# Kernel tuning notes

Measured on AMD Instinct MI355X. Metric: run time of the kernel, lower is better.

The kernel has to match this reference:

```python
import jax, jax.numpy as jnp
import numpy as np

IN_CAPS, IN_SIZE = 2401, 8
OUT_CAPS, OUT_SIZE = 8, 16
ROUTING_ITERS = 3


def squash(s, axis):
    mag_sq = jnp.sum(s * s, axis=axis, keepdims=True)
    mag = jnp.sqrt(mag_sq)
    return mag_sq / (1.0 + mag_sq) * (s / mag)


def setup_inputs() -> dict:
    key = jax.random.key(0)
    kx, kw = jax.random.split(key)
    B = 256
    x = jax.random.normal(kx, (B, IN_CAPS, IN_SIZE), dtype=jnp.float32)
    stdv = 1.0 / np.sqrt(IN_CAPS)
    W = jax.random.uniform(kw, (IN_CAPS, OUT_CAPS, OUT_SIZE, IN_SIZE),
                           dtype=jnp.float32, minval=-stdv, maxval=stdv)
    return {"x": x, "W": W}


def reference(x, W):
    # u_hat[b,i,o,c] = W[i,o,c,d] @ x[b,i,d]   -> [B, 2401, 8, 16]
    u_hat = jnp.einsum('iocd,bid->bioc', W, x)
    u_hat_det = jax.lax.stop_gradient(u_hat)

    b_ij = jnp.zeros((IN_CAPS, OUT_CAPS), dtype=x.dtype)
    v_j = None
    for it in range(ROUTING_ITERS):
        c_ij = jax.nn.softmax(b_ij, axis=1)  # softmax over out_capsules
        last = (it == ROUTING_ITERS - 1)
        u = u_hat if last else u_hat_det
        s_j = jnp.einsum('io,bioc->boc', c_ij, u)  # [B, 8, 16]
        v_j = squash(s_j, axis=-1)
        if not last:
            # agreement: mean over batch of <u_hat_i, v_j>
            a = jnp.einsum('bioc,boc->io', u_hat_det, v_j) / x.shape[0]
            b_ij = b_ij + a
    return v_j  # [B, 8, 16]
```

## Files before the change

kernel.cpp:

```cpp
#include <hip/hip_runtime.h>
#include <math.h>

#define IC     2401
#define BSZ    256
#define OC     8
#define CS     16
#define OCC    128
#define XROW   19208
#define KP     19264
#define KTILES 301
#define SNI    32

typedef __attribute__((ext_vector_type(8))) short short8;
typedef __attribute__((ext_vector_type(4))) float f32x4;

__device__ __forceinline__ unsigned short f2bf(float f) {
    union { float f; unsigned u; } v; v.f = f;
    const unsigned r = v.u + 0x7FFF + ((v.u >> 16) & 1);
    return (unsigned short)(r >> 16);
}
__device__ __forceinline__ float bf2f(unsigned short h) {
    union { unsigned u; float f; } v; v.u = ((unsigned)h) << 16;
    return v.f;
}
__device__ __forceinline__ void atomAddF32(float* p, float v) {
    (void)__hip_atomic_fetch_add(p, v, __ATOMIC_RELAXED, __HIP_MEMORY_SCOPE_AGENT);
}

__global__ __launch_bounds__(256)
void prep_kernel(const float* __restrict__ x, const float* __restrict__ W,
                 unsigned short* __restrict__ xT, unsigned short* __restrict__ xB,
                 unsigned short* __restrict__ Wbf, unsigned short* __restrict__ cwt,
                 float* __restrict__ s_acc_all)
{
    const int tid = threadIdx.x;
    if (blockIdx.x < 3) {
        float4* z = (float4*)(s_acc_all + (size_t)blockIdx.x * BSZ * OCC);
#pragma unroll
        for (int r = 0; r < 32; ++r)
            z[r * 256 + tid] = make_float4(0.f, 0.f, 0.f, 0.f);
    }
    if (blockIdx.x < 1204) {
        __shared__ float Ts[64 * 65];
        const int bg = blockIdx.x & 3;
        const int kt = blockIdx.x >> 2;
#pragma unroll
        for (int r = 0; r < 4; ++r) {
            const int flat = r * 256 + tid;
            const int b = flat >> 4, cq = flat & 15;
            const int col = kt * 64 + cq * 4;
            float4 v = make_float4(0.f, 0.f, 0.f, 0.f);
            if (col < XROW) v = *(const float4*)(x + (size_t)(bg * 64 + b) * XROW + col);
            *(float4*)&Ts[b * 65 + cq * 4] = v;
        }
        __syncthreads();
#pragma unroll
        for (int r = 0; r < 2; ++r) {
            const int flat = r * 256 + tid;
            const int rl = flat >> 3, bq = flat & 7;
            union { short8 v; unsigned short h[8]; } o;
#pragma unroll
            for (int j = 0; j < 8; ++j) o.h[j] = f2bf(Ts[(bq * 8 + j) * 65 + rl]);
            *(short8*)(xT + (size_t)(kt * 64 + rl) * 256 + bg * 64 + bq * 8) = o.v;
        }
#pragma unroll
        for (int r = 0; r < 2; ++r) {
            const int flat = r * 256 + tid;
            const int b = flat >> 3, g = flat & 7;
            union { short8 v; unsigned short h[8]; } o;
#pragma unroll
            for (int j = 0; j < 8; ++j) o.h[j] = f2bf(Ts[b * 65 + g * 8 + j]);
            *(short8*)(xB + (size_t)(bg * 64 + b) * KP + (size_t)kt * 64 + g * 8) = o.v;
        }
    } else {
        __shared__ float Ws[8 * 1032];
        const int i0 = (blockIdx.x - 1204) * 8;
#pragma unroll
        for (int r = 0; r < 8; ++r) {
            const int flat = r * 256 + tid;
            const int g = flat >> 8, rem = flat & 255;
            int gi = i0 + g; if (gi > 2400) gi = 2400;
            const float4 v = *(const float4*)(W + (size_t)gi * 1024 + rem * 4);
            *(float4*)&Ws[g * 1032 + rem * 4] = v;
        }
        __syncthreads();
#pragma unroll
        for (int r = 0; r < 4; ++r) {
            const int flat = r * 256 + tid;
            const int oc = flat >> 3, g = flat & 7;
            const int gi = i0 + g;
            union { short8 v; unsigned short h[8]; } w, c;
            if (gi <= 2400) {
                const float* wp = &Ws[g * 1032 + oc * 8];
#pragma unroll
                for (int j = 0; j < 8; ++j) {
                    w.h[j] = f2bf(wp[j]);
                    c.h[j] = f2bf(0.125f * wp[j]);
                }
            } else {
#pragma unroll
                for (int j = 0; j < 8; ++j) { w.h[j] = 0; c.h[j] = 0; }
            }
            *(short8*)(Wbf + (size_t)oc * KP + (size_t)gi * 8) = w.v;
            *(short8*)(cwt + (size_t)oc * KP + (size_t)gi * 8) = c.v;
        }
    }
}

__global__ __launch_bounds__(256, 2)
void s_gemm(const unsigned short* __restrict__ xB, const unsigned short* __restrict__ cwt,
            float* __restrict__ s_acc)
{
    __shared__ __align__(16) unsigned short Xs[64 * 64];
    __shared__ __align__(16) unsigned short Bs[128 * 64];
    const int tid = threadIdx.x;
    const int bg  = blockIdx.x, iy = blockIdx.y;
    const int b0  = bg * 64;
    const int ln  = tid & 63;
    const int mr  = ln & 15, qd = ln >> 4;
    const int mh  = (tid >> 6) & 1;
    const int nh  = tid >> 7;

    f32x4 acc[2][4];
#pragma unroll
    for (int a = 0; a < 2; ++a)
#pragma unroll
        for (int b = 0; b < 4; ++b) acc[a][b] = (f32x4){0.f, 0.f, 0.f, 0.f};

    const int srow = tid >> 3, scol = tid & 7;
    const int ssw  = (scol ^ (srow & 7)) * 8;
    const unsigned short* xp0 = xB  + (size_t)(b0 + srow) * KP + (size_t)scol * 8;
    const unsigned short* bp0 = cwt + (size_t)srow * KP + (size_t)scol * 8;

    short8 vx[2], vb[4];
    int kt = iy;
#pragma unroll
    for (int r = 0; r < 2; ++r) vx[r] = *(const short8*)(xp0 + (size_t)r * 32 * KP + (size_t)kt * 64);
#pragma unroll
    for (int r = 0; r < 4; ++r) vb[r] = *(const short8*)(bp0 + (size_t)r * 32 * KP + (size_t)kt * 64);

    while (true) {
        __syncthreads();
#pragma unroll
        for (int r = 0; r < 2; ++r) *(short8*)&Xs[(r * 32 + srow) * 64 + ssw] = vx[r];
#pragma unroll
        for (int r = 0; r < 4; ++r) *(short8*)&Bs[(r * 32 + srow) * 64 + ssw] = vb[r];
        const int ktn = kt + SNI;
        if (ktn < KTILES) {
#pragma unroll
            for (int r = 0; r < 2; ++r) vx[r] = *(const short8*)(xp0 + (size_t)r * 32 * KP + (size_t)ktn * 64);
#pragma unroll
            for (int r = 0; r < 4; ++r) vb[r] = *(const short8*)(bp0 + (size_t)r * 32 * KP + (size_t)ktn * 64);
        }
        __syncthreads();
#pragma unroll
        for (int kk = 0; kk < 2; ++kk) {
            const int csw = ((kk * 4 + qd) ^ (mr & 7)) * 8;
            const short8 a0 = *(const short8*)&Xs[(mh * 32 + mr) * 64 + csw];
            const short8 a1 = *(const short8*)&Xs[(mh * 32 + 16 + mr) * 64 + csw];
#pragma unroll
            for (int nt = 0; nt < 4; ++nt) {
                const short8 b = *(const short8*)&Bs[(nh * 64 + nt * 16 + mr) * 64 + csw];
                acc[0][nt] = __builtin_amdgcn_mfma_f32_16x16x32_bf16(a0, b, acc[0][nt], 0, 0, 0);
                acc[1][nt] = __builtin_amdgcn_mfma_f32_16x16x32_bf16(a1, b, acc[1][nt], 0, 0, 0);
            }
        }
        if (ktn >= KTILES) break;
        kt = ktn;
    }

    float* op = s_acc + (size_t)b0 * OCC;
#pragma unroll
    for (int mt = 0; mt < 2; ++mt)
#pragma unroll
        for (int nt = 0; nt < 4; ++nt)
#pragma unroll
            for (int r = 0; r < 4; ++r)
                atomAddF32(&op[(size_t)(mh * 32 + mt * 16 + qd * 4 + r) * OCC
                               + nh * 64 + nt * 16 + mr], acc[mt][nt][r]);
}

template<bool FIRST>
__global__ __launch_bounds__(256, 2)
void a_gemm(const unsigned short* __restrict__ xT, const float* __restrict__ s_acc,
            const unsigned short* __restrict__ Wbf, float* __restrict__ bij,
            unsigned short* __restrict__ cwt)
{
    __shared__ __align__(16) char smraw[128 * 68 * 4];
    unsigned short* As = (unsigned short*)smraw;
    unsigned short* Bx = (unsigned short*)(smraw + 16384);
    float* Hs = (float*)smraw;

    const int tid = threadIdx.x;
    const int i0  = blockIdx.x * 8;
    const int ln  = tid & 63, wv = tid >> 6;
    const int mr  = ln & 15, qd = ln >> 4;

    f32x4 acc[2][4];
#pragma unroll
    for (int a = 0; a < 2; ++a)
#pragma unroll
        for (int b = 0; b < 4; ++b) acc[a][b] = (f32x4){0.f, 0.f, 0.f, 0.f};

    const int srow = tid >> 3, scol = tid & 7;
    const int ssw  = (scol ^ (srow & 7)) * 8;
    const unsigned short* bp0 = xT + (size_t)(i0 * 8 + srow) * 256 + (size_t)scol * 8;

    short8 vbx[2];
#pragma unroll
    for (int r = 0; r < 2; ++r) vbx[r] = *(const short8*)(bp0 + (size_t)r * 32 * 256);

    for (int bc = 0; bc < 4; ++bc) {
        __syncthreads();
        {
            const int rr0 = tid * 2;
#pragma unroll
            for (int rv = 0; rv < 2; ++rv) {
                const int rr = rr0 + rv;
                const int bl = rr & 63;
                const int o  = rr >> 6;
                const float* sp = s_acc + (size_t)(bc * 64 + bl) * OCC + o * 16;
                const float4 s0 = *(const float4*)(sp);
                const float4 s1 = *(const float4*)(sp + 4);
                const float4 s2 = *(const float4*)(sp + 8);
                const float4 s3 = *(const float4*)(sp + 12);
                float ms = s0.x*s0.x + s0.y*s0.y + s0.z*s0.z + s0.w*s0.w
                         + s1.x*s1.x + s1.y*s1.y + s1.z*s1.z + s1.w*s1.w
                         + s2.x*s2.x + s2.y*s2.y + s2.z*s2.z + s2.w*s2.w
                         + s3.x*s3.x + s3.y*s3.y + s3.z*s3.z + s3.w*s3.w;
                const float scale = sqrtf(ms) / (1.0f + ms);
                float vv[16] = { s0.x, s0.y, s0.z, s0.w, s1.x, s1.y, s1.z, s1.w,
                                 s2.x, s2.y, s2.z, s2.w, s3.x, s3.y, s3.z, s3.w };
                const int blq = bl >> 3, blr = bl & 7;
#pragma unroll
                for (int c = 0; c < 16; ++c) {
                    const int oc = o * 16 + c;
                    As[oc * 64 + ((blq ^ (oc & 7)) * 8) + blr] = f2bf(vv[c] * scale);
                }
            }
        }
#pragma unroll
        for (int r = 0; r < 2; ++r) *(short8*)&Bx[(r * 32 + srow) * 64 + ssw] = vbx[r];
        if (bc < 3) {
#pragma unroll
            for (int r = 0; r < 2; ++r) vbx[r] = *(const short8*)(bp0 + (size_t)r * 32 * 256 + (bc + 1) * 64);
        }
        __syncthreads();
#pragma unroll
        for (int kk = 0; kk < 2; ++kk) {
            const int csw = ((kk * 4 + qd) ^ (mr & 7)) * 8;
#pragma unroll
            for (int nt = 0; nt < 4; ++nt) {
                const short8 b = *(const short8*)&Bx[(nt * 16 + mr) * 64 + csw];
#pragma unroll
                for (int mt = 0; mt < 2; ++mt) {
                    const short8 a = *(const short8*)&As[((wv * 2 + mt) * 16 + mr) * 64 + csw];
                    acc[mt][nt] = __builtin_amdgcn_mfma_f32_16x16x32_bf16(a, b, acc[mt][nt], 0, 0, 0);
                }
            }
        }
    }

    __syncthreads();
#pragma unroll
    for (int mt = 0; mt < 2; ++mt)
#pragma unroll
        for (int nt = 0; nt < 4; ++nt)
#pragma unroll
            for (int r = 0; r < 4; ++r)
                Hs[((wv * 2 + mt) * 16 + qd * 4 + r) * 68 + nt * 16 + mr] = acc[mt][nt][r];
    __syncthreads();

    const int ch = tid & 3, oo = (tid >> 2) & 7, il = tid >> 5;
    const int ival = i0 + il;
    const int gi = (ival < IC) ? ival : IC - 1;
    const unsigned short* Wt = Wbf + (size_t)(oo * 16 + ch * 4) * KP + (size_t)gi * 8;

    float wreg[4][8];
#pragma unroll
    for (int c = 0; c < 4; ++c) {
        union { short8 v; unsigned short h[8]; } uw;
        uw.v = *(const short8*)(Wt + (size_t)c * KP);
#pragma unroll
        for (int j = 0; j < 8; ++j) wreg[c][j] = bf2f(uw.h[j]);
    }
    float p = 0.0f;
#pragma unroll
    for (int c = 0; c < 4; ++c) {
        const float* hr = &Hs[(oo * 16 + ch * 4 + c) * 68 + il * 8];
        const float4 h0 = *(const float4*)hr;
        const float4 h1 = *(const float4*)(hr + 4);
        p = fmaf(wreg[c][0], h0.x, p); p = fmaf(wreg[c][1], h0.y, p);
        p = fmaf(wreg[c][2], h0.z, p); p = fmaf(wreg[c][3], h0.w, p);
        p = fmaf(wreg[c][4], h1.x, p); p = fmaf(wreg[c][5], h1.y, p);
        p = fmaf(wreg[c][6], h1.z, p); p = fmaf(wreg[c][7], h1.w, p);
    }
    p += __shfl_xor(p, 1); p += __shfl_xor(p, 2);
    const float anew = p * (1.0f / 256.0f);
    float bv = anew;
    if (!FIRST) bv += bij[gi * 8 + oo];
    float mx = bv;
    mx = fmaxf(mx, __shfl_xor(mx, 4));
    mx = fmaxf(mx, __shfl_xor(mx, 8));
    mx = fmaxf(mx, __shfl_xor(mx, 16));
    const float e = expf(bv - mx);
    float ss = e;
    ss += __shfl_xor(ss, 4); ss += __shfl_xor(ss, 8); ss += __shfl_xor(ss, 16);
    float cv = e / ss;
    if (ival >= IC) cv = 0.0f;
    if (ch == 0 && ival < IC) bij[ival * 8 + oo] = bv;
#pragma unroll
    for (int c = 0; c < 4; ++c) {
        union { short8 v; unsigned short h[8]; } o;
#pragma unroll
        for (int j = 0; j < 8; ++j) o.h[j] = f2bf(cv * wreg[c][j]);
        *(short8*)(cwt + (size_t)(oo * 16 + ch * 4 + c) * KP + (size_t)ival * 8) = o.v;
    }
}

__global__ __launch_bounds__(256)
void squash_out(const float* __restrict__ s_acc, float* __restrict__ out)
{
    const int row = blockIdx.x * 256 + threadIdx.x;
    const float* sp = s_acc + (size_t)(row >> 3) * OCC + (row & 7) * 16;
    const float4 s0 = *(const float4*)(sp);
    const float4 s1 = *(const float4*)(sp + 4);
    const float4 s2 = *(const float4*)(sp + 8);
    const float4 s3 = *(const float4*)(sp + 12);
    const float ms = s0.x*s0.x + s0.y*s0.y + s0.z*s0.z + s0.w*s0.w
                   + s1.x*s1.x + s1.y*s1.y + s1.z*s1.z + s1.w*s1.w
                   + s2.x*s2.x + s2.y*s2.y + s2.z*s2.z + s2.w*s2.w
                   + s3.x*s3.x + s3.y*s3.y + s3.z*s3.z + s3.w*s3.w;
    const float scale = sqrtf(ms) / (1.0f + ms);
    float4* op = (float4*)(out + (size_t)row * 16);
    op[0] = make_float4(s0.x*scale, s0.y*scale, s0.z*scale, s0.w*scale);
    op[1] = make_float4(s1.x*scale, s1.y*scale, s1.z*scale, s1.w*scale);
    op[2] = make_float4(s2.x*scale, s2.y*scale, s2.z*scale, s2.w*scale);
    op[3] = make_float4(s3.x*scale, s3.y*scale, s3.z*scale, s3.w*scale);
}

extern "C" void kernel_launch(void* const* d_in, const int* in_sizes, int n_in,
                              void* d_out, int out_size, void* d_ws, size_t ws_size,
                              hipStream_t stream)
{
    const float* x = (const float*)d_in[0];
    const float* W = (const float*)d_in[1];
    float* out = (float*)d_out;

    char* p = (char*)d_ws;
    float*          s_acc = (float*)p;          p += (size_t)3 * BSZ * OCC * 4;
    unsigned short* xT    = (unsigned short*)p; p += (size_t)KP * 256 * 2;
    unsigned short* xB    = (unsigned short*)p; p += (size_t)256 * KP * 2;
    unsigned short* Wbf   = (unsigned short*)p; p += (size_t)128 * KP * 2;
    unsigned short* cwt   = (unsigned short*)p; p += (size_t)128 * KP * 2;
    float*          bij   = (float*)p;

    float* s0 = s_acc;
    float* s1 = s_acc + (size_t)BSZ * OCC;
    float* s2 = s_acc + (size_t)2 * BSZ * OCC;

    const dim3 sgrid(4, SNI);

    prep_kernel<<<1505, 256, 0, stream>>>(x, W, xT, xB, Wbf, cwt, s_acc);

    s_gemm<<<sgrid, 256, 0, stream>>>(xB, cwt, s0);
    a_gemm<true><<<KTILES, 256, 0, stream>>>(xT, s0, Wbf, bij, cwt);
    s_gemm<<<sgrid, 256, 0, stream>>>(xB, cwt, s1);
    a_gemm<false><<<KTILES, 256, 0, stream>>>(xT, s1, Wbf, bij, cwt);
    s_gemm<<<sgrid, 256, 0, stream>>>(xB, cwt, s2);
    squash_out<<<8, 256, 0, stream>>>(s2, out);
}
```

Before: 138.9 us.

## Double block size to 512 threads in s_gemm and a_gemm, doubling split-K

Both GEMM kernels move from 256 to 512 threads per block. Each wave now computes a single 16-row M tile instead of two, which halves the per-thread accumulators and the per-thread global loads. The s_gemm split-K factor doubles from 32 to 64 to put more blocks in flight, at the cost of twice as many atomic adds into the output. In a_gemm the final W·H dot product is split across two thread halves and combined through an LDS reduction, adding an extra synchronisation and shared-memory traffic in return for more parallel threads.

```diff
diff --git a/kernel.cpp b/kernel.cpp
--- a/kernel.cpp
+++ b/kernel.cpp
@@ -9,7 +9,7 @@
 #define XROW   19208
 #define KP     19264
 #define KTILES 301
-#define SNI    32
+#define SNI    64
 
 typedef __attribute__((ext_vector_type(8))) short short8;
 typedef __attribute__((ext_vector_type(4))) float f32x4;
@@ -107,7 +107,7 @@
     }
 }
 
-__global__ __launch_bounds__(256, 2)
+__global__ __launch_bounds__(512)
 void s_gemm(const unsigned short* __restrict__ xB, const unsigned short* __restrict__ cwt,
             float* __restrict__ s_acc)
 {
@@ -118,51 +118,45 @@
     const int b0  = bg * 64;
     const int ln  = tid & 63;
     const int mr  = ln & 15, qd = ln >> 4;
-    const int mh  = (tid >> 6) & 1;
-    const int nh  = tid >> 7;
-
-    f32x4 acc[2][4];
-#pragma unroll
-    for (int a = 0; a < 2; ++a)
-#pragma unroll
-        for (int b = 0; b < 4; ++b) acc[a][b] = (f32x4){0.f, 0.f, 0.f, 0.f};
+    const int wv  = tid >> 6;
+    const int mq  = wv & 3;
+    const int nh  = wv >> 2;
+
+    f32x4 acc[4];
+#pragma unroll
+    for (int b = 0; b < 4; ++b) acc[b] = (f32x4){0.f, 0.f, 0.f, 0.f};
 
     const int srow = tid >> 3, scol = tid & 7;
     const int ssw  = (scol ^ (srow & 7)) * 8;
     const unsigned short* xp0 = xB  + (size_t)(b0 + srow) * KP + (size_t)scol * 8;
     const unsigned short* bp0 = cwt + (size_t)srow * KP + (size_t)scol * 8;
 
-    short8 vx[2], vb[4];
+    short8 vx, vb[2];
     int kt = iy;
-#pragma unroll
-    for (int r = 0; r < 2; ++r) vx[r] = *(const short8*)(xp0 + (size_t)r * 32 * KP + (size_t)kt * 64);
-#pragma unroll
-    for (int r = 0; r < 4; ++r) vb[r] = *(const short8*)(bp0 + (size_t)r * 32 * KP + (size_t)kt * 64);
+    vx = *(const short8*)(xp0 + (size_t)kt * 64);
+#pragma unroll
+    for (int r = 0; r < 2; ++r) vb[r] = *(const short8*)(bp0 + (size_t)r * 64 * KP + (size_t)kt * 64);
 
     while (true) {
         __syncthreads();
-#pragma unroll
-        for (int r = 0; r < 2; ++r) *(short8*)&Xs[(r * 32 + srow) * 64 + ssw] = vx[r];
-#pragma unroll
-        for (int r = 0; r < 4; ++r) *(short8*)&Bs[(r * 32 + srow) * 64 + ssw] = vb[r];
+        *(short8*)&Xs[srow * 64 + ssw] = vx;
+#pragma unroll
+        for (int r = 0; r < 2; ++r) *(short8*)&Bs[(r * 64 + srow) * 64 + ssw] = vb[r];
         const int ktn = kt + SNI;
         if (ktn < KTILES) {
-#pragma unroll
-            for (int r = 0; r < 2; ++r) vx[r] = *(const short8*)(xp0 + (size_t)r * 32 * KP + (size_t)ktn * 64);
-#pragma unroll
-            for (int r = 0; r < 4; ++r) vb[r] = *(const short8*)(bp0 + (size_t)r * 32 * KP + (size_t)ktn * 64);
+            vx = *(const short8*)(xp0 + (size_t)ktn * 64);
+#pragma unroll
+            for (int r = 0; r < 2; ++r) vb[r] = *(const short8*)(bp0 + (size_t)r * 64 * KP + (size_t)ktn * 64);
         }
         __syncthreads();
 #pragma unroll
         for (int kk = 0; kk < 2; ++kk) {
             const int csw = ((kk * 4 + qd) ^ (mr & 7)) * 8;
-            const short8 a0 = *(const short8*)&Xs[(mh * 32 + mr) * 64 + csw];
-            const short8 a1 = *(const short8*)&Xs[(mh * 32 + 16 + mr) * 64 + csw];
+            const short8 a = *(const short8*)&Xs[(mq * 16 + mr) * 64 + csw];
 #pragma unroll
             for (int nt = 0; nt < 4; ++nt) {
                 const short8 b = *(const short8*)&Bs[(nh * 64 + nt * 16 + mr) * 64 + csw];
-                acc[0][nt] = __builtin_amdgcn_mfma_f32_16x16x32_bf16(a0, b, acc[0][nt], 0, 0, 0);
-                acc[1][nt] = __builtin_amdgcn_mfma_f32_16x16x32_bf16(a1, b, acc[1][nt], 0, 0, 0);
+                acc[nt] = __builtin_amdgcn_mfma_f32_16x16x32_bf16(a, b, acc[nt], 0, 0, 0);
             }
         }
         if (ktn >= KTILES) break;
@@ -171,80 +165,67 @@
 
     float* op = s_acc + (size_t)b0 * OCC;
 #pragma unroll
-    for (int mt = 0; mt < 2; ++mt)
-#pragma unroll
-        for (int nt = 0; nt < 4; ++nt)
-#pragma unroll
-            for (int r = 0; r < 4; ++r)
-                atomAddF32(&op[(size_t)(mh * 32 + mt * 16 + qd * 4 + r) * OCC
-                               + nh * 64 + nt * 16 + mr], acc[mt][nt][r]);
+    for (int nt = 0; nt < 4; ++nt)
+#pragma unroll
+        for (int r = 0; r < 4; ++r)
+            atomAddF32(&op[(size_t)(mq * 16 + qd * 4 + r) * OCC + nh * 64 + nt * 16 + mr],
+                       acc[nt][r]);
 }
 
 template<bool FIRST>
-__global__ __launch_bounds__(256, 2)
+__global__ __launch_bounds__(512)
 void a_gemm(const unsigned short* __restrict__ xT, const float* __restrict__ s_acc,
             const unsigned short* __restrict__ Wbf, float* __restrict__ bij,
             unsigned short* __restrict__ cwt)
 {
-    __shared__ __align__(16) char smraw[128 * 68 * 4];
+    __shared__ __align__(16) char smraw[36352];
     unsigned short* As = (unsigned short*)smraw;
     unsigned short* Bx = (unsigned short*)(smraw + 16384);
-    float* Hs = (float*)smraw;
+    float* Hs  = (float*)smraw;
+    float* red = (float*)(smraw + 34816);
+    float* cvs = (float*)(smraw + 35840);
 
     const int tid = threadIdx.x;
     const int i0  = blockIdx.x * 8;
     const int ln  = tid & 63, wv = tid >> 6;
     const int mr  = ln & 15, qd = ln >> 4;
 
-    f32x4 acc[2][4];
-#pragma unroll
-    for (int a = 0; a < 2; ++a)
-#pragma unroll
-        for (int b = 0; b < 4; ++b) acc[a][b] = (f32x4){0.f, 0.f, 0.f, 0.f};
+    f32x4 acc[4];
+#pragma unroll
+    for (int b = 0; b < 4; ++b) acc[b] = (f32x4){0.f, 0.f, 0.f, 0.f};
 
     const int srow = tid >> 3, scol = tid & 7;
     const int ssw  = (scol ^ (srow & 7)) * 8;
     const unsigned short* bp0 = xT + (size_t)(i0 * 8 + srow) * 256 + (size_t)scol * 8;
 
-    short8 vbx[2];
-#pragma unroll
-    for (int r = 0; r < 2; ++r) vbx[r] = *(const short8*)(bp0 + (size_t)r * 32 * 256);
+    short8 vbx = *(const short8*)(bp0);
+
+    const int bl = tid & 63, o = tid >> 6;
+    const int blq = bl >> 3, blr = bl & 7;
 
     for (int bc = 0; bc < 4; ++bc) {
         __syncthreads();
         {
-            const int rr0 = tid * 2;
-#pragma unroll
-            for (int rv = 0; rv < 2; ++rv) {
-                const int rr = rr0 + rv;
-                const int bl = rr & 63;
-                const int o  = rr >> 6;
-                const float* sp = s_acc + (size_t)(bc * 64 + bl) * OCC + o * 16;
-                const float4 s0 = *(const float4*)(sp);
-                const float4 s1 = *(const float4*)(sp + 4);
-                const float4 s2 = *(const float4*)(sp + 8);
-                const float4 s3 = *(const float4*)(sp + 12);
-                float ms = s0.x*s0.x + s0.y*s0.y + s0.z*s0.z + s0.w*s0.w
-                         + s1.x*s1.x + s1.y*s1.y + s1.z*s1.z + s1.w*s1.w
-                         + s2.x*s2.x + s2.y*s2.y + s2.z*s2.z + s2.w*s2.w
-                         + s3.x*s3.x + s3.y*s3.y + s3.z*s3.z + s3.w*s3.w;
-                const float scale = sqrtf(ms) / (1.0f + ms);
-                float vv[16] = { s0.x, s0.y, s0.z, s0.w, s1.x, s1.y, s1.z, s1.w,
-                                 s2.x, s2.y, s2.z, s2.w, s3.x, s3.y, s3.z, s3.w };
-                const int blq = bl >> 3, blr = bl & 7;
-#pragma unroll
-                for (int c = 0; c < 16; ++c) {
-                    const int oc = o * 16 + c;
-                    As[oc * 64 + ((blq ^ (oc & 7)) * 8) + blr] = f2bf(vv[c] * scale);
-                }
+            const float* sp = s_acc + (size_t)(bc * 64 + bl) * OCC + o * 16;
+            const float4 s0 = *(const float4*)(sp);
+            const float4 s1 = *(const float4*)(sp + 4);
+            const float4 s2 = *(const float4*)(sp + 8);
+            const float4 s3 = *(const float4*)(sp + 12);
+            float ms = s0.x*s0.x + s0.y*s0.y + s0.z*s0.z + s0.w*s0.w
+                     + s1.x*s1.x + s1.y*s1.y + s1.z*s1.z + s1.w*s1.w
+                     + s2.x*s2.x + s2.y*s2.y + s2.z*s2.z + s2.w*s2.w
+                     + s3.x*s3.x + s3.y*s3.y + s3.z*s3.z + s3.w*s3.w;
+            const float scale = sqrtf(ms) / (1.0f + ms);
+            float vv[16] = { s0.x, s0.y, s0.z, s0.w, s1.x, s1.y, s1.z, s1.w,
+                             s2.x, s2.y, s2.z, s2.w, s3.x, s3.y, s3.z, s3.w };
+#pragma unroll
+            for (int c = 0; c < 16; ++c) {
+                const int oc = o * 16 + c;
+                As[oc * 64 + ((blq ^ (oc & 7)) * 8) + blr] = f2bf(vv[c] * scale);
             }
         }
-#pragma unroll
-        for (int r = 0; r < 2; ++r) *(short8*)&Bx[(r * 32 + srow) * 64 + ssw] = vbx[r];
-        if (bc < 3) {
-#pragma unroll
-            for (int r = 0; r < 2; ++r) vbx[r] = *(const short8*)(bp0 + (size_t)r * 32 * 256 + (bc + 1) * 64);
-        }
+        *(short8*)&Bx[srow * 64 + ssw] = vbx;
+        if (bc < 3) vbx = *(const short8*)(bp0 + (bc + 1) * 64);
         __syncthreads();
 #pragma unroll
         for (int kk = 0; kk < 2; ++kk) {
@@ -252,33 +233,28 @@
 #pragma unroll
             for (int nt = 0; nt < 4; ++nt) {
                 const short8 b = *(const short8*)&Bx[(nt * 16 + mr) * 64 + csw];
-#pragma unroll
-                for (int mt = 0; mt < 2; ++mt) {
-                    const short8 a = *(const short8*)&As[((wv * 2 + mt) * 16 + mr) * 64 + csw];
-                    acc[mt][nt] = __builtin_amdgcn_mfma_f32_16x16x32_bf16(a, b, acc[mt][nt], 0, 0, 0);
-                }
+                const short8 a = *(const short8*)&As[(wv * 16 + mr) * 64 + csw];
+                acc[nt] = __builtin_amdgcn_mfma_f32_16x16x32_bf16(a, b, acc[nt], 0, 0, 0);
             }
         }
     }
 
     __syncthreads();
 #pragma unroll
-    for (int mt = 0; mt < 2; ++mt)
-#pragma unroll
-        for (int nt = 0; nt < 4; ++nt)
-#pragma unroll
-            for (int r = 0; r < 4; ++r)
-                Hs[((wv * 2 + mt) * 16 + qd * 4 + r) * 68 + nt * 16 + mr] = acc[mt][nt][r];
+    for (int nt = 0; nt < 4; ++nt)
+#pragma unroll
+        for (int r = 0; r < 4; ++r)
+            Hs[(wv * 16 + qd * 4 + r) * 68 + nt * 16 + mr] = acc[nt][r];
     __syncthreads();
 
-    const int ch = tid & 3, oo = (tid >> 2) & 7, il = tid >> 5;
+    const int ch = tid & 3, oo = (tid >> 2) & 7, il = (tid >> 5) & 7, cc = tid >> 8;
     const int ival = i0 + il;
     const int gi = (ival < IC) ? ival : IC - 1;
-    const unsigned short* Wt = Wbf + (size_t)(oo * 16 + ch * 4) * KP + (size_t)gi * 8;
-
-    float wreg[4][8];
-#pragma unroll
-    for (int c = 0; c < 4; ++c) {
+    const unsigned short* Wt = Wbf + (size_t)(oo * 16 + ch * 4 + cc * 2) * KP + (size_t)gi * 8;
+
+    float wreg[2][8];
+#pragma unroll
+    for (int c = 0; c < 2; ++c) {
         union { short8 v; unsigned short h[8]; } uw;
         uw.v = *(const short8*)(Wt + (size_t)c * KP);
 #pragma unroll
@@ -286,8 +262,8 @@
     }
     float p = 0.0f;
 #pragma unroll
-    for (int c = 0; c < 4; ++c) {
-        const float* hr = &Hs[(oo * 16 + ch * 4 + c) * 68 + il * 8];
+    for (int c = 0; c < 2; ++c) {
+        const float* hr = &Hs[(oo * 16 + ch * 4 + cc * 2 + c) * 68 + il * 8];
         const float4 h0 = *(const float4*)hr;
         const float4 h1 = *(const float4*)(hr + 4);
         p = fmaf(wreg[c][0], h0.x, p); p = fmaf(wreg[c][1], h0.y, p);
@@ -296,25 +272,35 @@
         p = fmaf(wreg[c][6], h1.z, p); p = fmaf(wreg[c][7], h1.w, p);
     }
     p += __shfl_xor(p, 1); p += __shfl_xor(p, 2);
-    const float anew = p * (1.0f / 256.0f);
-    float bv = anew;
-    if (!FIRST) bv += bij[gi * 8 + oo];
-    float mx = bv;
-    mx = fmaxf(mx, __shfl_xor(mx, 4));
-    mx = fmaxf(mx, __shfl_xor(mx, 8));
-    mx = fmaxf(mx, __shfl_xor(mx, 16));
-    const float e = expf(bv - mx);
-    float ss = e;
-    ss += __shfl_xor(ss, 4); ss += __shfl_xor(ss, 8); ss += __shfl_xor(ss, 16);
-    float cv = e / ss;
-    if (ival >= IC) cv = 0.0f;
-    if (ch == 0 && ival < IC) bij[ival * 8 + oo] = bv;
-#pragma unroll
-    for (int c = 0; c < 4; ++c) {
-        union { short8 v; unsigned short h[8]; } o;
-#pragma unroll
-        for (int j = 0; j < 8; ++j) o.h[j] = f2bf(cv * wreg[c][j]);
-        *(short8*)(cwt + (size_t)(oo * 16 + ch * 4 + c) * KP + (size_t)ival * 8) = o.v;
+    if (cc) red[tid & 255] = p;
+    __syncthreads();
+    if (!cc) {
+        p += red[tid];
+        const float anew = p * (1.0f / 256.0f);
+        float bv = anew;
+        if (!FIRST) bv += bij[gi * 8 + oo];
+        float mx = bv;
+        mx = fmaxf(mx, __shfl_xor(mx, 4));
+        mx = fmaxf(mx, __shfl_xor(mx, 8));
+        mx = fmaxf(mx, __shfl_xor(mx, 16));
+        const float e = expf(bv - mx);
+        float ss = e;
+        ss += __shfl_xor(ss, 4); ss += __shfl_xor(ss, 8); ss += __shfl_xor(ss, 16);
+        float cv = e / ss;
+        if (ival >= IC) cv = 0.0f;
+        if (ch == 0) {
+            if (ival < IC) bij[ival * 8 + oo] = bv;
+            cvs[il * 8 + oo] = cv;
+        }
+    }
+    __syncthreads();
+    const float cv = cvs[il * 8 + oo];
+#pragma unroll
+    for (int c = 0; c < 2; ++c) {
+        union { short8 v; unsigned short h[8]; } ov;
+#pragma unroll
+        for (int j = 0; j < 8; ++j) ov.h[j] = f2bf(cv * wreg[c][j]);
+        *(short8*)(cwt + (size_t)(oo * 16 + ch * 4 + cc * 2 + c) * KP + (size_t)ival * 8) = ov.v;
     }
 }
 
@@ -363,10 +349,10 @@
 
     prep_kernel<<<1505, 256, 0, stream>>>(x, W, xT, xB, Wbf, cwt, s_acc);
 
-    s_gemm<<<sgrid, 256, 0, stream>>>(xB, cwt, s0);
-    a_gemm<true><<<KTILES, 256, 0, stream>>>(xT, s0, Wbf, bij, cwt);
-    s_gemm<<<sgrid, 256, 0, stream>>>(xB, cwt, s1);
-    a_gemm<false><<<KTILES, 256, 0, stream>>>(xT, s1, Wbf, bij, cwt);
-    s_gemm<<<sgrid, 256, 0, stream>>>(xB, cwt, s2);
+    s_gemm<<<sgrid, 512, 0, stream>>>(xB, cwt, s0);
+    a_gemm<true><<<KTILES, 512, 0, stream>>>(xT, s0, Wbf, bij, cwt);
+    s_gemm<<<sgrid, 512, 0, stream>>>(xB, cwt, s1);
+    a_gemm<false><<<KTILES, 512, 0, stream>>>(xT, s1, Wbf, bij, cwt);
+    s_gemm<<<sgrid, 512, 0, stream>>>(xB, cwt, s2);
     squash_out<<<8, 256, 0, stream>>>(s2, out);
 }
```

New measurement: 142.4 us. 1.02x slower.
